# Optimization experiments

Hardware: AMD Instinct MI355X
Metric: run time of the kernel (lower is better)

## Reference

```python
import jax, jax.numpy as jnp
import numpy as np

B, N, F_IN, M, U = 2, 2048, 128, 8, 64


def setup_inputs() -> dict:
    key = jax.random.key(0)
    k1, k2, k3, k4 = jax.random.split(key, 4)
    seq_data = jax.random.normal(k1, (B, N, F_IN), dtype=jnp.float32)
    # weighted multi-layer digraph adjacency (B, N_to, N_from, M)
    graph = jax.random.uniform(k2, (B, N, N, M), dtype=jnp.float32)
    e_weight = jax.random.normal(k3, (F_IN, U), dtype=jnp.float32) * (1.0 / np.sqrt(F_IN))
    v_weight = jax.random.normal(k4, (F_IN, M, U), dtype=jnp.float32) * (1.0 / np.sqrt(F_IN))
    return {"seq_data": seq_data, "graph": graph, "e_weight": e_weight, "v_weight": v_weight}


def reference(seq_data, graph, e_weight, v_weight):
    # beta = seq_data @ e_weight : (B, N, U)
    beta = jnp.einsum('bnf,fu->bnu', seq_data, e_weight)
    # _batch_dot(graph, beta, axes=(2,1)) -> einsum 'bijm,bju->bimu'
    out = jnp.einsum('bijm,bju->bimu', graph, beta)
    # node self-loop term: reshape-free einsum of v_weight (F_in, M, U)
    alpha = jnp.einsum('bnf,fmu->bnmu', seq_data, v_weight)
    return jax.nn.sigmoid(out + alpha)  # (B, N, M, U)
```

## Files before the change

### kernel.cpp

```cpp
#include <hip/hip_runtime.h>
#include <cmath>

#define N_ 2048
#define F_ 128
#define M_ 8
#define U_ 64

typedef _Float16 f16;
typedef _Float16 f16x2 __attribute__((ext_vector_type(2)));
typedef _Float16 f16x8 __attribute__((ext_vector_type(8)));
typedef float f32x4 __attribute__((ext_vector_type(4)));

#define BK 32
#define RS 40
#define NCH (N_ / BK)

__global__ __launch_bounds__(256) void k_pre(const float* __restrict__ seq,
                                             const float* __restrict__ ew,
                                             const float* __restrict__ vw,
                                             f16* __restrict__ bh,
                                             float* __restrict__ out) {
  __shared__ float smem[16 * 132];
  const int t = threadIdx.x;

  if (blockIdx.x < 512) {
    const int q    = t & 15;
    const int g    = t >> 4;
    const int r    = g & 7;
    const int mh   = g >> 3;
    const int row0 = blockIdx.x * 8;
    {
      float4 v = *(const float4*)(seq + (size_t)row0 * F_ + t * 4);
      *(float4*)&smem[t * 4] = v;
    }
    __syncthreads();
    float acc[4][4] = {};
    const float* wbase = vw + mh * 4 * 64 + q * 4;
#pragma unroll 4
    for (int f = 0; f < F_; ++f) {
      float s = smem[r * F_ + f];
      const float* wf = wbase + (size_t)f * 512;
#pragma unroll
      for (int mm = 0; mm < 4; ++mm) {
        float4 wv = *(const float4*)(wf + mm * 64);
        acc[mm][0] = fmaf(s, wv.x, acc[mm][0]);
        acc[mm][1] = fmaf(s, wv.y, acc[mm][1]);
        acc[mm][2] = fmaf(s, wv.z, acc[mm][2]);
        acc[mm][3] = fmaf(s, wv.w, acc[mm][3]);
      }
    }
    float* o = out + (size_t)(row0 + r) * 512 + mh * 4 * 64 + q * 4;
#pragma unroll
    for (int mm = 0; mm < 4; ++mm) {
      float4 res;
      res.x = acc[mm][0]; res.y = acc[mm][1];
      res.z = acc[mm][2]; res.w = acc[mm][3];
      *(float4*)(o + mm * 64) = res;
    }
  } else {
    const int lane = t & 63;
    const int wv   = t >> 6;
    const int row0 = (blockIdx.x - 512) * 16;
#pragma unroll
    for (int k = 0; k < 2; ++k) {
      int id = t + k * 256;
      int r = id >> 5, f4 = id & 31;
      float4 v = *(const float4*)(seq + (size_t)(row0 + r) * F_ + f4 * 4);
      *(float4*)&smem[r * 132 + f4 * 4] = v;
    }
    __syncthreads();
    const int r0 = wv * 4;
    float acc[4] = {0.f, 0.f, 0.f, 0.f};
#pragma unroll 8
    for (int f = 0; f < F_; ++f) {
      float e = ew[f * U_ + lane];
#pragma unroll
      for (int r = 0; r < 4; ++r)
        acc[r] = fmaf(smem[(r0 + r) * 132 + f], e, acc[r]);
    }
#pragma unroll
    for (int r = 0; r < 4; ++r) {
      int row = row0 + r0 + r;
      int b = row >> 11, n = row & (N_ - 1);
      size_t idx = ((size_t)(b * U_ + lane)) * N_ + n;
      bh[idx] = (f16)acc[r];
    }
  }
}

__global__ __launch_bounds__(256, 2) void k_main(const float* __restrict__ graph,
                                                 const f16* __restrict__ betah,
                                                 float* __restrict__ out) {
  __shared__ f16 Ah[2][64 * RS];
  __shared__ f16 Al[2][64 * RS];
  __shared__ f16 Bh[2][64 * RS];

  const int t    = threadIdx.x;
  const int w    = t >> 6;
  const int lane = t & 63;
  const int l15  = lane & 15;
  const int quad = lane >> 4;
  const int wr   = w >> 1;
  const int wc   = w & 1;

  const int bx = blockIdx.x;
  const int b  = bx >> 8;
  const int rb = bx & 255;

  const int iA = t >> 5;
  const int r5 = t & 31;
  const int jp = r5 >> 1;
  const int mh = r5 & 1;
  const int uB = t >> 2;
  const int pB = t & 3;

  const float* gA = graph + ((size_t)(b * N_ + rb * 8 + iA)) * (N_ * M_) + mh * 4;
  const f16* bhp = betah + ((size_t)(b * U_ + uB)) * N_ + pB * 8;

  f32x4 acc[2][2] = {{f32x4{0.f, 0.f, 0.f, 0.f}, f32x4{0.f, 0.f, 0.f, 0.f}},
                     {f32x4{0.f, 0.f, 0.f, 0.f}, f32x4{0.f, 0.f, 0.f, 0.f}}};

  float4 ra0_0, ra1_0; uint4 rbh_0;
  float4 ra0_1, ra1_1; uint4 rbh_1;

#define LOADC(c, S)                                                       \
  do {                                                                    \
    const float* g_ = gA + (size_t)((c) * BK + jp * 2) * M_;              \
    ra0_##S = *(const float4*)g_;                                         \
    ra1_##S = *(const float4*)(g_ + M_);                                  \
    rbh_##S = *(const uint4*)(bhp + (c) * BK);                            \
  } while (0)

#define WRITEC(buf, S)                                                    \
  do {                                                                    \
    float g0s[4] = {ra0_##S.x, ra0_##S.y, ra0_##S.z, ra0_##S.w};          \
    float g1s[4] = {ra1_##S.x, ra1_##S.y, ra1_##S.z, ra1_##S.w};          \
    _Pragma("unroll") for (int mw = 0; mw < 4; ++mw) {                    \
      float g0 = g0s[mw], g1 = g1s[mw];                                   \
      f16 h0 = (f16)g0, h1 = (f16)g1;                                     \
      f16 l0 = (f16)(g0 - (float)h0), l1 = (f16)(g1 - (float)h1);         \
      int r_ = iA * 8 + mh * 4 + mw;                                      \
      f16x2 hv; hv[0] = h0; hv[1] = h1;                                   \
      f16x2 lv; lv[0] = l0; lv[1] = l1;                                   \
      *(f16x2*)&Ah[buf][r_ * RS + jp * 2] = hv;                           \
      *(f16x2*)&Al[buf][r_ * RS + jp * 2] = lv;                           \
    }                                                                     \
    *(uint4*)&Bh[buf][uB * RS + pB * 8] = rbh_##S;                        \
  } while (0)

#define COMPUTE(buf)                                                      \
  do {                                                                    \
    f16x8 bhf[2];                                                         \
    _Pragma("unroll") for (int nt = 0; nt < 2; ++nt) {                    \
      const int bb_ = (wc * 32 + nt * 16 + l15) * RS + quad * 8;          \
      bhf[nt] = *(const f16x8*)&Bh[buf][bb_];                             \
    }                                                                     \
    _Pragma("unroll") for (int mt = 0; mt < 2; ++mt) {                    \
      const int ab_ = (wr * 32 + mt * 16 + l15) * RS + quad * 8;          \
      f16x8 ah = *(const f16x8*)&Ah[buf][ab_];                            \
      f16x8 al = *(const f16x8*)&Al[buf][ab_];                            \
      _Pragma("unroll") for (int nt = 0; nt < 2; ++nt) {                  \
        acc[mt][nt] = __builtin_amdgcn_mfma_f32_16x16x32_f16(ah, bhf[nt], acc[mt][nt], 0, 0, 0); \
        acc[mt][nt] = __builtin_amdgcn_mfma_f32_16x16x32_f16(al, bhf[nt], acc[mt][nt], 0, 0, 0); \
      }                                                                   \
    }                                                                     \
  } while (0)

#define BAR()                                                             \
  do {                                                                    \
    asm volatile("s_waitcnt lgkmcnt(0)" ::: "memory");                    \
    __builtin_amdgcn_s_barrier();                                         \
    asm volatile("" ::: "memory");                                        \
  } while (0)

  LOADC(0, 0);
  WRITEC(0, 0);
  LOADC(1, 1);
  BAR();

  for (int cc = 0; cc < NCH - 4; cc += 2) {
    COMPUTE(0);
    LOADC(cc + 2, 0);
    WRITEC(1, 1);
    BAR();
    COMPUTE(1);
    LOADC(cc + 3, 1);
    WRITEC(0, 0);
    BAR();
  }

  COMPUTE(0);
  LOADC(NCH - 2, 0);
  WRITEC(1, 1);
  BAR();
  COMPUTE(1);
  LOADC(NCH - 1, 1);
  WRITEC(0, 0);
  BAR();
  COMPUTE(0);
  WRITEC(1, 1);
  BAR();
  COMPUTE(1);

  const int rowbase = rb * 64 + wr * 32 + quad * 4;
#pragma unroll
  for (int mt = 0; mt < 2; ++mt) {
#pragma unroll
    for (int nt = 0; nt < 2; ++nt) {
      const int u = wc * 32 + nt * 16 + l15;
#pragma unroll
      for (int reg = 0; reg < 4; ++reg) {
        size_t idx = ((size_t)(b * 16384 + rowbase + mt * 16 + reg)) * U_ + u;
        float x = acc[mt][nt][reg] + out[idx];
        out[idx] = 1.0f / (1.0f + __expf(-x));
      }
    }
  }
#undef LOADC
#undef WRITEC
#undef COMPUTE
#undef BAR
}

extern "C" void kernel_launch(void* const* d_in, const int* in_sizes, int n_in,
                              void* d_out, int out_size, void* d_ws, size_t ws_size,
                              hipStream_t stream) {
  const float* seq   = (const float*)d_in[0];
  const float* graph = (const float*)d_in[1];
  const float* ew    = (const float*)d_in[2];
  const float* vw    = (const float*)d_in[3];
  float* out = (float*)d_out;

  f16* betah = (f16*)d_ws;

  hipLaunchKernelGGL(k_pre,  dim3(768), dim3(256), 0, stream, seq, ew, vw, betah, out);
  hipLaunchKernelGGL(k_main, dim3(512), dim3(256), 0, stream, graph, betah, out);
}
```

Measured before the change: 397.6 us.

## Fuse alpha self-loop term into main kernel epilogue via MFMA

Moves the alpha = seq·v_weight computation out of the pre-kernel and into the tail of the main graph-aggregation kernel. Each block now stages its 8 seq rows in fp16 in LDS, computes alpha with f16 MFMAs, and adds it from LDS before the sigmoid. This removes the fp32 round trip of alpha through the output buffer and makes the pre-kernel smaller. In exchange it adds fp16 rounding on seq and v_weight, extra LDS use that may reduce occupancy, and uncoalesced per-element v_weight loads in every block.

```diff
diff --git a/kernel.cpp b/kernel.cpp
--- a/kernel.cpp
+++ b/kernel.cpp
@@ -13,87 +13,54 @@
 
 #define BK 32
 #define RS 40
+#define RS2 136
+#define AS 66
 #define NCH (N_ / BK)
 
 __global__ __launch_bounds__(256) void k_pre(const float* __restrict__ seq,
                                              const float* __restrict__ ew,
-                                             const float* __restrict__ vw,
-                                             f16* __restrict__ bh,
-                                             float* __restrict__ out) {
+                                             f16* __restrict__ bh) {
   __shared__ float smem[16 * 132];
-  const int t = threadIdx.x;
-
-  if (blockIdx.x < 512) {
-    const int q    = t & 15;
-    const int g    = t >> 4;
-    const int r    = g & 7;
-    const int mh   = g >> 3;
-    const int row0 = blockIdx.x * 8;
-    {
-      float4 v = *(const float4*)(seq + (size_t)row0 * F_ + t * 4);
-      *(float4*)&smem[t * 4] = v;
-    }
-    __syncthreads();
-    float acc[4][4] = {};
-    const float* wbase = vw + mh * 4 * 64 + q * 4;
-#pragma unroll 4
-    for (int f = 0; f < F_; ++f) {
-      float s = smem[r * F_ + f];
-      const float* wf = wbase + (size_t)f * 512;
-#pragma unroll
-      for (int mm = 0; mm < 4; ++mm) {
-        float4 wv = *(const float4*)(wf + mm * 64);
-        acc[mm][0] = fmaf(s, wv.x, acc[mm][0]);
-        acc[mm][1] = fmaf(s, wv.y, acc[mm][1]);
-        acc[mm][2] = fmaf(s, wv.z, acc[mm][2]);
-        acc[mm][3] = fmaf(s, wv.w, acc[mm][3]);
-      }
-    }
-    float* o = out + (size_t)(row0 + r) * 512 + mh * 4 * 64 + q * 4;
-#pragma unroll
-    for (int mm = 0; mm < 4; ++mm) {
-      float4 res;
-      res.x = acc[mm][0]; res.y = acc[mm][1];
-      res.z = acc[mm][2]; res.w = acc[mm][3];
-      *(float4*)(o + mm * 64) = res;
-    }
-  } else {
-    const int lane = t & 63;
-    const int wv   = t >> 6;
-    const int row0 = (blockIdx.x - 512) * 16;
-#pragma unroll
-    for (int k = 0; k < 2; ++k) {
-      int id = t + k * 256;
-      int r = id >> 5, f4 = id & 31;
-      float4 v = *(const float4*)(seq + (size_t)(row0 + r) * F_ + f4 * 4);
-      *(float4*)&smem[r * 132 + f4 * 4] = v;
-    }
-    __syncthreads();
-    const int r0 = wv * 4;
-    float acc[4] = {0.f, 0.f, 0.f, 0.f};
+  const int t    = threadIdx.x;
+  const int lane = t & 63;
+  const int wv   = t >> 6;
+  const int row0 = blockIdx.x * 16;
+#pragma unroll
+  for (int k = 0; k < 2; ++k) {
+    int id = t + k * 256;
+    int r = id >> 5, f4 = id & 31;
+    float4 v = *(const float4*)(seq + (size_t)(row0 + r) * F_ + f4 * 4);
+    *(float4*)&smem[r * 132 + f4 * 4] = v;
+  }
+  __syncthreads();
+  const int r0 = wv * 4;
+  float acc[4] = {0.f, 0.f, 0.f, 0.f};
 #pragma unroll 8
-    for (int f = 0; f < F_; ++f) {
-      float e = ew[f * U_ + lane];
-#pragma unroll
-      for (int r = 0; r < 4; ++r)
-        acc[r] = fmaf(smem[(r0 + r) * 132 + f], e, acc[r]);
-    }
-#pragma unroll
-    for (int r = 0; r < 4; ++r) {
-      int row = row0 + r0 + r;
-      int b = row >> 11, n = row & (N_ - 1);
-      size_t idx = ((size_t)(b * U_ + lane)) * N_ + n;
-      bh[idx] = (f16)acc[r];
-    }
+  for (int f = 0; f < F_; ++f) {
+    float e = ew[f * U_ + lane];
+#pragma unroll
+    for (int r = 0; r < 4; ++r)
+      acc[r] = fmaf(smem[(r0 + r) * 132 + f], e, acc[r]);
+  }
+#pragma unroll
+  for (int r = 0; r < 4; ++r) {
+    int row = row0 + r0 + r;
+    int b = row >> 11, n = row & (N_ - 1);
+    size_t idx = ((size_t)(b * U_ + lane)) * N_ + n;
+    bh[idx] = (f16)acc[r];
   }
 }
 
 __global__ __launch_bounds__(256, 2) void k_main(const float* __restrict__ graph,
+                                                 const float* __restrict__ seq,
+                                                 const float* __restrict__ vw,
                                                  const f16* __restrict__ betah,
                                                  float* __restrict__ out) {
   __shared__ f16 Ah[2][64 * RS];
   __shared__ f16 Al[2][64 * RS];
   __shared__ f16 Bh[2][64 * RS];
+  __shared__ f16 seqh[16 * RS2];
+  __shared__ float alds[64 * AS];
 
   const int t    = threadIdx.x;
   const int w    = t >> 6;
@@ -116,6 +83,19 @@
 
   const float* gA = graph + ((size_t)(b * N_ + rb * 8 + iA)) * (N_ * M_) + mh * 4;
   const f16* bhp = betah + ((size_t)(b * U_ + uB)) * N_ + pB * 8;
+
+  {
+    const int r  = t >> 5;
+    const int f4 = (t & 31) * 4;
+    float4 v = *(const float4*)(seq + ((size_t)(b * N_ + rb * 8 + r)) * F_ + f4);
+    f16x2 p0; p0[0] = (f16)v.x; p0[1] = (f16)v.y;
+    f16x2 p1; p1[0] = (f16)v.z; p1[1] = (f16)v.w;
+    *(f16x2*)&seqh[r * RS2 + f4]     = p0;
+    *(f16x2*)&seqh[r * RS2 + f4 + 2] = p1;
+    f16x2 z; z[0] = (f16)0.f; z[1] = (f16)0.f;
+    *(f16x2*)&seqh[(r + 8) * RS2 + f4]     = z;
+    *(f16x2*)&seqh[(r + 8) * RS2 + f4 + 2] = z;
+  }
 
   f32x4 acc[2][2] = {{f32x4{0.f, 0.f, 0.f, 0.f}, f32x4{0.f, 0.f, 0.f, 0.f}},
                      {f32x4{0.f, 0.f, 0.f, 0.f}, f32x4{0.f, 0.f, 0.f, 0.f}}};
@@ -202,6 +182,40 @@
   BAR();
   COMPUTE(1);
 
+  {
+    f32x4 acca[2][4] = {{f32x4{0.f,0.f,0.f,0.f}, f32x4{0.f,0.f,0.f,0.f},
+                         f32x4{0.f,0.f,0.f,0.f}, f32x4{0.f,0.f,0.f,0.f}},
+                        {f32x4{0.f,0.f,0.f,0.f}, f32x4{0.f,0.f,0.f,0.f},
+                         f32x4{0.f,0.f,0.f,0.f}, f32x4{0.f,0.f,0.f,0.f}}};
+    const int m0 = w * 2;
+#pragma unroll
+    for (int ks = 0; ks < 4; ++ks) {
+      f16x8 af = *(const f16x8*)&seqh[l15 * RS2 + ks * 32 + quad * 8];
+#pragma unroll
+      for (int mi = 0; mi < 2; ++mi) {
+        const float* vwp = vw + (size_t)(ks * 32 + quad * 8) * 512 + (m0 + mi) * 64 + l15;
+#pragma unroll
+        for (int nt2 = 0; nt2 < 4; ++nt2) {
+          f16x8 bf;
+#pragma unroll
+          for (int j = 0; j < 8; ++j)
+            bf[j] = (f16)vwp[(size_t)j * 512 + nt2 * 16];
+          acca[mi][nt2] = __builtin_amdgcn_mfma_f32_16x16x32_f16(af, bf, acca[mi][nt2], 0, 0, 0);
+        }
+      }
+    }
+    if (quad < 2) {
+#pragma unroll
+      for (int mi = 0; mi < 2; ++mi)
+#pragma unroll
+        for (int nt2 = 0; nt2 < 4; ++nt2)
+#pragma unroll
+          for (int reg = 0; reg < 4; ++reg)
+            alds[((quad * 4 + reg) * 8 + m0 + mi) * AS + nt2 * 16 + l15] = acca[mi][nt2][reg];
+    }
+  }
+  BAR();
+
   const int rowbase = rb * 64 + wr * 32 + quad * 4;
 #pragma unroll
   for (int mt = 0; mt < 2; ++mt) {
@@ -210,8 +224,9 @@
       const int u = wc * 32 + nt * 16 + l15;
 #pragma unroll
       for (int reg = 0; reg < 4; ++reg) {
+        const int lrow = wr * 32 + mt * 16 + quad * 4 + reg;
         size_t idx = ((size_t)(b * 16384 + rowbase + mt * 16 + reg)) * U_ + u;
-        float x = acc[mt][nt][reg] + out[idx];
+        float x = acc[mt][nt][reg] + alds[lrow * AS + u];
         out[idx] = 1.0f / (1.0f + __expf(-x));
       }
     }
@@ -233,6 +248,6 @@
 
   f16* betah = (f16*)d_ws;
 
-  hipLaunchKernelGGL(k_pre,  dim3(768), dim3(256), 0, stream, seq, ew, vw, betah, out);
-  hipLaunchKernelGGL(k_main, dim3(512), dim3(256), 0, stream, graph, betah, out);
+  hipLaunchKernelGGL(k_pre,  dim3(256), dim3(256), 0, stream, seq, ew, betah);
+  hipLaunchKernelGGL(k_main, dim3(512), dim3(256), 0, stream, graph, seq, vw, betah, out);
 }
```

Measured after the change: 374.7 us. 1.06x faster.
